# Optimization experiments

Hardware: AMD Instinct MI355X
Metric: run time of the kernel (lower is better)

The kernel has to match this reference:

```python
import jax, jax.numpy as jnp
import numpy as np

N = 50000          # total nodes (100 graphs x 500 nodes)
E = 500000         # total edges
G = 100            # graphs in batch
NODES_PER_GRAPH = 500
N_PROT = 400       # protein nodes per graph (rest are ligand)
H = 128            # hidden_dim
PN, LN, EA = 35, 11, 4
L = 4              # num EGNN layers
EPS = 1e-5


def setup_inputs() -> dict:
    key = jax.random.key(0)
    ks = jax.random.split(key, 40)
    s = 0.1
    inp = {}
    inp["x"] = jax.random.normal(ks[0], (N, PN), jnp.float32)
    inp["pos"] = jax.random.normal(ks[1], (N, 3), jnp.float32)
    inp["edge_index"] = jax.random.randint(ks[2], (2, E), 0, N, jnp.int32)
    inp["edge_attr"] = jax.random.normal(ks[3], (E, EA), jnp.float32)
    node_id = jnp.arange(N, dtype=jnp.int32)
    inp["batch"] = node_id // NODES_PER_GRAPH
    inp["is_protein"] = (node_id % NODES_PER_GRAPH) < N_PROT
    # input projections + batchnorm params
    inp["Wp"] = jax.random.normal(ks[4], (PN, H), jnp.float32) * s
    inp["bp"] = jnp.zeros((H,), jnp.float32)
    inp["Wl"] = jax.random.normal(ks[5], (LN, H), jnp.float32) * s
    inp["bl"] = jnp.zeros((H,), jnp.float32)
    inp["bn_gamma"] = jnp.ones((H,), jnp.float32)
    inp["bn_beta"] = jnp.zeros((H,), jnp.float32)
    # stacked per-layer EGNN params
    din_e = 2 * H + 1 + EA  # 261
    inp["e_w1"] = jax.random.normal(ks[6], (L, din_e, H), jnp.float32) * s
    inp["e_b1"] = jnp.zeros((L, H), jnp.float32)
    inp["e_w2"] = jax.random.normal(ks[7], (L, H, H), jnp.float32) * s
    inp["e_b2"] = jnp.zeros((L, H), jnp.float32)
    inp["c_w1"] = jax.random.normal(ks[8], (L, H, H), jnp.float32) * s
    inp["c_b1"] = jnp.zeros((L, H), jnp.float32)
    inp["c_w2"] = jax.random.normal(ks[9], (L, H, 1), jnp.float32) * s
    inp["n_w1"] = jax.random.normal(ks[10], (L, 2 * H, H), jnp.float32) * s
    inp["n_b1"] = jnp.zeros((L, H), jnp.float32)
    inp["n_w2"] = jax.random.normal(ks[11], (L, H, H), jnp.float32) * s
    inp["n_b2"] = jnp.zeros((L, H), jnp.float32)
    # readout head: 2H -> 128 -> 64 -> 1
    inp["h1_w"] = jax.random.normal(ks[12], (2 * H, 128), jnp.float32) * s
    inp["h1_b"] = jnp.zeros((128,), jnp.float32)
    inp["h2_w"] = jax.random.normal(ks[13], (128, 64), jnp.float32) * s
    inp["h2_b"] = jnp.zeros((64,), jnp.float32)
    inp["h3_w"] = jax.random.normal(ks[14], (64, 1), jnp.float32) * s
    inp["h3_b"] = jnp.zeros((1,), jnp.float32)
    return inp


def reference(x, pos, edge_index, edge_attr, batch, is_protein,
              Wp, bp, Wl, bl, bn_gamma, bn_beta,
              e_w1, e_b1, e_w2, e_b2, c_w1, c_b1, c_w2,
              n_w1, n_b1, n_w2, n_b2,
              h1_w, h1_b, h2_w, h2_b, h3_w, h3_b):
    # --- node projection (protein vs ligand feature slices) ---
    h_prot = x[:, :PN] @ Wp + bp              # [N, H]
    h_lig = x[:, :LN] @ Wl + bl               # [N, H]
    h = jnp.where(is_protein[:, None], h_prot, h_lig)
    # BatchNorm1d (training-mode batch statistics)
    mu = h.mean(axis=0)
    var = h.var(axis=0)
    h = (h - mu) / jnp.sqrt(var + EPS) * bn_gamma + bn_beta

    row, col = edge_index[0], edge_index[1]   # aggregate messages at row (target)
    deg = jax.ops.segment_sum(jnp.ones((row.shape[0],), h.dtype), row, num_segments=N)
    deg = jnp.maximum(deg, 1.0)[:, None]

    for l in range(e_w1.shape[0]):
        rel = pos[row] - pos[col]                                  # [E, 3]
        d2 = jnp.sum(rel * rel, axis=-1, keepdims=True)            # [E, 1]
        feat = jnp.concatenate([h[row], h[col], d2, edge_attr], -1)  # [E, 261]
        m = jax.nn.silu(jax.nn.silu(feat @ e_w1[l] + e_b1[l]) @ e_w2[l] + e_b2[l])  # [E, H]
        # coordinate update (mean aggregation of gated relative positions)
        w = jax.nn.silu(m @ c_w1[l] + c_b1[l]) @ c_w2[l]           # [E, 1]
        pos = pos + jax.ops.segment_sum(rel * w, row, num_segments=N) / deg
        # node update with residual
        agg = jax.ops.segment_sum(m, row, num_segments=N)          # [N, H]
        upd = jax.nn.silu(jnp.concatenate([h, agg], -1) @ n_w1[l] + n_b1[l]) @ n_w2[l] + n_b2[l]
        h = h + upd

    # --- sum||mean pooling per graph ---
    gsum = jax.ops.segment_sum(h, batch, num_segments=G)           # [G, H]
    cnt = jax.ops.segment_sum(jnp.ones((h.shape[0],), h.dtype), batch, num_segments=G)
    gfeat = jnp.concatenate([gsum, gsum / jnp.maximum(cnt, 1.0)[:, None]], -1)  # [G, 2H]

    # --- MLP head (dropout inactive at inference) ---
    z = jax.nn.relu(gfeat @ h1_w + h1_b)
    z = jax.nn.relu(z @ h2_w + h2_b)
    return z @ h3_w + h3_b                                          # [G, 1]
```

## Files before the change

### kernel.cpp

```cpp
#include <hip/hip_runtime.h>
#include <math.h>

#define N_NODES 50000
#define N_EDGES 500000
#define G_GRAPHS 100
#define NPG 500
#define NPROT 400
#define H 128
#define PN 35
#define LN 11
#define DIN 261
#define EB2 32
#define FS2 136
#define T2S 132
#define NBN 64
#define NB2 32
#define CST 264
#define NB 16
#define NCHUNK 49
#define EPSV 1e-5f

typedef __attribute__((ext_vector_type(8))) short bf8_t;
typedef __attribute__((ext_vector_type(4))) short bf4_t;
typedef __attribute__((ext_vector_type(4))) float f4_t;

__device__ __forceinline__ float silu_f(float x) {
    return x / (1.0f + __expf(-x));
}
__device__ __forceinline__ short f2b(float f) {
    __bf16 b = (__bf16)f;
    return __builtin_bit_cast(short, b);
}
__device__ __forceinline__ float b2f(short s) {
    unsigned u = ((unsigned)(unsigned short)s) << 16;
    return __builtin_bit_cast(float, u);
}

__global__ void wprep_frag_kernel(const float* __restrict__ src, short* __restrict__ dstH,
                                  short* __restrict__ dstL, int Ksrc, int nkb, int koff) {
    int idx = blockIdx.x * 256 + threadIdx.x;
    int per_l = nkb * 8 * 64 * 8;
    int total = 4 * per_l;
    if (idx >= total) return;
    int l = idx / per_l;
    int rem = idx - l * per_l;
    int j = rem & 7;
    int lane = (rem >> 3) & 63;
    int nt = (rem >> 9) & 7;
    int kb = rem >> 12;
    int ln = lane & 15, quad = lane >> 4;
    int n = nt * 16 + ln;
    int k = koff + kb * 32 + quad * 8 + j;
    float v = (k < Ksrc) ? src[((size_t)l * Ksrc + k) * H + n] : 0.0f;
    short hi = f2b(v);
    dstH[idx] = hi;
    dstL[idx] = f2b(v - b2f(hi));
}

__global__ void hist_kernel(const int* __restrict__ ei, int* __restrict__ cnt)
{
    int e = blockIdx.x * 256 + threadIdx.x;
    if (e < N_EDGES) atomicAdd(&cnt[ei[e]], 1);
}

__global__ __launch_bounds__(256) void bsum_kernel(const int* __restrict__ cnt, int* __restrict__ bsum)
{
    __shared__ int red[4];
    int tid = threadIdx.x;
    int i0 = blockIdx.x * 1024 + tid * 4;
    int s = 0;
    #pragma unroll
    for (int j = 0; j < 4; j++) {
        int i = i0 + j;
        if (i < N_NODES) s += cnt[i];
    }
    #pragma unroll
    for (int off = 32; off > 0; off >>= 1) s += __shfl_down(s, off, 64);
    if ((tid & 63) == 0) red[tid >> 6] = s;
    __syncthreads();
    if (tid == 0) bsum[blockIdx.x] = red[0] + red[1] + red[2] + red[3];
}

__global__ void scanb_kernel(const int* __restrict__ bsum, int* __restrict__ boff)
{
    if (threadIdx.x == 0) {
        int acc = 0;
        for (int i = 0; i < NCHUNK; i++) { boff[i] = acc; acc += bsum[i]; }
    }
}

__global__ __launch_bounds__(256) void scanc_kernel(const int* __restrict__ cnt,
                                                    const int* __restrict__ boff,
                                                    int* __restrict__ base)
{
    __shared__ int ts[256];
    int tid = threadIdx.x;
    int b = blockIdx.x;
    int i0 = b * 1024 + tid * 4;
    int v0 = (i0 + 0 < N_NODES) ? cnt[i0 + 0] : 0;
    int v1 = (i0 + 1 < N_NODES) ? cnt[i0 + 1] : 0;
    int v2 = (i0 + 2 < N_NODES) ? cnt[i0 + 2] : 0;
    int v3 = (i0 + 3 < N_NODES) ? cnt[i0 + 3] : 0;
    int s0 = v0, s1 = s0 + v1, s2 = s1 + v2, s3 = s2 + v3;
    ts[tid] = s3;
    __syncthreads();
    for (int off = 1; off < 256; off <<= 1) {
        int t = (tid >= off) ? ts[tid - off] : 0;
        __syncthreads();
        ts[tid] += t;
        __syncthreads();
    }
    int excl = ((tid > 0) ? ts[tid - 1] : 0) + boff[b];
    if (i0 + 0 < N_NODES) base[i0 + 0] = excl;
    if (i0 + 1 < N_NODES) base[i0 + 1] = excl + s0;
    if (i0 + 2 < N_NODES) base[i0 + 2] = excl + s1;
    if (i0 + 3 < N_NODES) base[i0 + 3] = excl + s2;
}

__global__ void scatter_kernel(const int* __restrict__ ei, const int* __restrict__ base,
                               int* __restrict__ cursor, int* __restrict__ perm,
                               int* __restrict__ rowsS)
{
    int e = blockIdx.x * 256 + threadIdx.x;
    if (e < N_EDGES) {
        int r = ei[e];
        int p = atomicAdd(&cursor[r], 1);
        int d = base[r] + p;
        perm[d] = e;
        rowsS[d] = r;
    }
}

__global__ void deg_from_cnt_kernel(const int* __restrict__ cnt, float* __restrict__ deg)
{
    int i = blockIdx.x * 256 + threadIdx.x;
    if (i < N_NODES) deg[i] = (float)cnt[i];
}

__global__ __launch_bounds__(128) void proj_kernel(
    const float* __restrict__ x, const float* __restrict__ Wp, const float* __restrict__ bp,
    const float* __restrict__ Wl, const float* __restrict__ bl, float* __restrict__ h)
{
    __shared__ float xs[NB][36];
    int tid = threadIdx.x;
    int n0 = blockIdx.x * NB;
    for (int idx = tid; idx < NB * PN; idx += 128) {
        int n = idx / PN, k = idx % PN;
        xs[n][k] = x[(size_t)(n0 + n) * PN + k];
    }
    __syncthreads();
    for (int n = 0; n < NB; n++) {
        int node = n0 + n;
        bool isp = (node % NPG) < NPROT;
        float acc;
        if (isp) {
            acc = bp[tid];
            for (int k = 0; k < PN; k++) acc = fmaf(xs[n][k], Wp[k * H + tid], acc);
        } else {
            acc = bl[tid];
            for (int k = 0; k < LN; k++) acc = fmaf(xs[n][k], Wl[k * H + tid], acc);
        }
        h[(size_t)node * H + tid] = acc;
    }
}

__global__ __launch_bounds__(128) void bn_stats_kernel(const float* __restrict__ h, float* __restrict__ bnS)
{
    int tid = threadIdx.x;
    size_t base = (size_t)blockIdx.x * NPG * H;
    float s1 = 0.f, s2 = 0.f;
    for (int i = 0; i < NPG; i++) {
        float v = h[base + (size_t)i * H + tid];
        s1 += v; s2 += v * v;
    }
    atomicAdd(&bnS[tid], s1);
    atomicAdd(&bnS[H + tid], s2);
}

__global__ void bn_final_kernel(const float* __restrict__ bnS, const float* __restrict__ gamma,
                                const float* __restrict__ beta, float* __restrict__ bnP)
{
    int j = threadIdx.x;
    float mu = bnS[j] / (float)N_NODES;
    float var = bnS[H + j] / (float)N_NODES - mu * mu;
    float inv = rsqrtf(var + EPSV);
    float sc = gamma[j] * inv;
    bnP[j] = sc;
    bnP[H + j] = beta[j] - mu * sc;
}

__global__ __launch_bounds__(256) void bn_apply_kernel(float* __restrict__ h, const float* __restrict__ bnP)
{
    int idx = blockIdx.x * 256 + threadIdx.x;
    float4 v = ((float4*)h)[idx];
    int j4 = (idx & 31) * 4;
    v.x = fmaf(v.x, bnP[j4 + 0], bnP[H + j4 + 0]);
    v.y = fmaf(v.y, bnP[j4 + 1], bnP[H + j4 + 1]);
    v.z = fmaf(v.z, bnP[j4 + 2], bnP[H + j4 + 2]);
    v.w = fmaf(v.w, bnP[j4 + 3], bnP[H + j4 + 3]);
    ((float4*)h)[idx] = v;
}

__device__ __forceinline__ void mm_hl2(
    const short* fH, const short* fL, int stride,
    const short* __restrict__ WH, const short* __restrict__ WL,
    int nkb, int nt0, int lane, int ln, int quad, f4_t acc[2][2])
{
    #pragma unroll
    for (int mi = 0; mi < 2; mi++)
        #pragma unroll
        for (int ni = 0; ni < 2; ni++) acc[mi][ni] = (f4_t)(0.0f);
    for (int kb = 0; kb < nkb; kb++) {
        int k0 = kb * 32 + quad * 8;
        bf8_t ah0 = *(const bf8_t*)&fH[(ln) * stride + k0];
        bf8_t al0 = *(const bf8_t*)&fL[(ln) * stride + k0];
        bf8_t ah1 = *(const bf8_t*)&fH[(16 + ln) * stride + k0];
        bf8_t al1 = *(const bf8_t*)&fL[(16 + ln) * stride + k0];
        #pragma unroll
        for (int ni = 0; ni < 2; ni++) {
            int off = ((kb * 8 + nt0 + ni) * 64 + lane) * 8;
            bf8_t bh = *(const bf8_t*)&WH[off];
            bf8_t bl = *(const bf8_t*)&WL[off];
            acc[0][ni] = __builtin_amdgcn_mfma_f32_16x16x32_bf16(ah0, bh, acc[0][ni], 0, 0, 0);
            acc[0][ni] = __builtin_amdgcn_mfma_f32_16x16x32_bf16(al0, bh, acc[0][ni], 0, 0, 0);
            acc[0][ni] = __builtin_amdgcn_mfma_f32_16x16x32_bf16(ah0, bl, acc[0][ni], 0, 0, 0);
            acc[1][ni] = __builtin_amdgcn_mfma_f32_16x16x32_bf16(ah1, bh, acc[1][ni], 0, 0, 0);
            acc[1][ni] = __builtin_amdgcn_mfma_f32_16x16x32_bf16(al1, bh, acc[1][ni], 0, 0, 0);
            acc[1][ni] = __builtin_amdgcn_mfma_f32_16x16x32_bf16(ah1, bl, acc[1][ni], 0, 0, 0);
        }
    }
}

__device__ __forceinline__ void mm_h2t(
    const short* fH, int stride,
    const short* __restrict__ WH, const short* __restrict__ WL,
    int nkb, int nt0, int lane, int ln, int quad, f4_t acc[2][2])
{
    #pragma unroll
    for (int mi = 0; mi < 2; mi++)
        #pragma unroll
        for (int ni = 0; ni < 2; ni++) acc[mi][ni] = (f4_t)(0.0f);
    for (int kb = 0; kb < nkb; kb++) {
        int k0 = kb * 32 + quad * 8;
        bf8_t ah0 = *(const bf8_t*)&fH[(ln) * stride + k0];
        bf8_t ah1 = *(const bf8_t*)&fH[(16 + ln) * stride + k0];
        #pragma unroll
        for (int ni = 0; ni < 2; ni++) {
            int off = ((kb * 8 + nt0 + ni) * 64 + lane) * 8;
            bf8_t bh = *(const bf8_t*)&WH[off];
            bf8_t bl = *(const bf8_t*)&WL[off];
            acc[0][ni] = __builtin_amdgcn_mfma_f32_16x16x32_bf16(ah0, bh, acc[0][ni], 0, 0, 0);
            acc[0][ni] = __builtin_amdgcn_mfma_f32_16x16x32_bf16(ah0, bl, acc[0][ni], 0, 0, 0);
            acc[1][ni] = __builtin_amdgcn_mfma_f32_16x16x32_bf16(ah1, bh, acc[1][ni], 0, 0, 0);
            acc[1][ni] = __builtin_amdgcn_mfma_f32_16x16x32_bf16(ah1, bl, acc[1][ni], 0, 0, 0);
        }
    }
}

__device__ __forceinline__ void mm_hl4(
    const short* fH, const short* fL, int stride,
    const short* __restrict__ WH, const short* __restrict__ WL,
    int nkb, int nt, int lane, int ln, int quad, f4_t acc[4])
{
    #pragma unroll
    for (int mi = 0; mi < 4; mi++) acc[mi] = (f4_t)(0.0f);
    for (int kb = 0; kb < nkb; kb++) {
        int k0 = kb * 32 + quad * 8;
        int off = ((kb * 8 + nt) * 64 + lane) * 8;
        bf8_t bh = *(const bf8_t*)&WH[off];
        bf8_t bl = *(const bf8_t*)&WL[off];
        #pragma unroll
        for (int mi = 0; mi < 4; mi++) {
            bf8_t ah = *(const bf8_t*)&fH[(mi * 16 + ln) * stride + k0];
            bf8_t al = *(const bf8_t*)&fL[(mi * 16 + ln) * stride + k0];
            acc[mi] = __builtin_amdgcn_mfma_f32_16x16x32_bf16(ah, bh, acc[mi], 0, 0, 0);
            acc[mi] = __builtin_amdgcn_mfma_f32_16x16x32_bf16(al, bh, acc[mi], 0, 0, 0);
            acc[mi] = __builtin_amdgcn_mfma_f32_16x16x32_bf16(ah, bl, acc[mi], 0, 0, 0);
        }
    }
}

__global__ __launch_bounds__(512, 4) void p12_kernel(
    const float* __restrict__ h,
    const short* __restrict__ Ah, const short* __restrict__ Al,
    const short* __restrict__ Bh, const short* __restrict__ Bl,
    float* __restrict__ P1, float* __restrict__ P2)
{
    __shared__ __align__(16) short fH[NBN * FS2];
    __shared__ __align__(16) short fL[NBN * FS2];
    int tid = threadIdx.x;
    int n0 = blockIdx.x * NBN;

    for (int i = tid; i < NBN * (H / 4); i += 512) {
        int nidx = i >> 5, chunk = i & 31;
        int node = n0 + nidx;
        if (node >= N_NODES) node = N_NODES - 1;
        f4_t v = *(const f4_t*)&h[(size_t)node * H + chunk * 4];
        bf4_t hi, lo;
        #pragma unroll
        for (int j = 0; j < 4; j++) {
            hi[j] = f2b(v[j]);
            lo[j] = f2b(v[j] - b2f(hi[j]));
        }
        *(bf4_t*)&fH[nidx * FS2 + chunk * 4] = hi;
        *(bf4_t*)&fL[nidx * FS2 + chunk * 4] = lo;
    }
    __syncthreads();

    int lane = tid & 63;
    int nt = tid >> 6;
    int ln = lane & 15, quad = lane >> 4;

    f4_t accA[4], accB[4];
    #pragma unroll
    for (int mi = 0; mi < 4; mi++) { accA[mi] = (f4_t)(0.0f); accB[mi] = (f4_t)(0.0f); }
    for (int kb = 0; kb < 4; kb++) {
        int k0 = kb * 32 + quad * 8;
        int off = ((kb * 8 + nt) * 64 + lane) * 8;
        bf8_t bhA = *(const bf8_t*)&Ah[off];
        bf8_t blA = *(const bf8_t*)&Al[off];
        bf8_t bhB = *(const bf8_t*)&Bh[off];
        bf8_t blB = *(const bf8_t*)&Bl[off];
        #pragma unroll
        for (int mi = 0; mi < 4; mi++) {
            bf8_t ah = *(const bf8_t*)&fH[(mi * 16 + ln) * FS2 + k0];
            bf8_t al = *(const bf8_t*)&fL[(mi * 16 + ln) * FS2 + k0];
            accA[mi] = __builtin_amdgcn_mfma_f32_16x16x32_bf16(ah, bhA, accA[mi], 0, 0, 0);
            accA[mi] = __builtin_amdgcn_mfma_f32_16x16x32_bf16(al, bhA, accA[mi], 0, 0, 0);
            accA[mi] = __builtin_amdgcn_mfma_f32_16x16x32_bf16(ah, blA, accA[mi], 0, 0, 0);
            accB[mi] = __builtin_amdgcn_mfma_f32_16x16x32_bf16(ah, bhB, accB[mi], 0, 0, 0);
            accB[mi] = __builtin_amdgcn_mfma_f32_16x16x32_bf16(al, bhB, accB[mi], 0, 0, 0);
            accB[mi] = __builtin_amdgcn_mfma_f32_16x16x32_bf16(ah, blB, accB[mi], 0, 0, 0);
        }
    }
    int n = nt * 16 + ln;
    #pragma unroll
    for (int mi = 0; mi < 4; mi++) {
        #pragma unroll
        for (int r = 0; r < 4; r++) {
            int node = n0 + mi * 16 + quad * 4 + r;
            if (node < N_NODES) {
                P1[(size_t)node * H + n] = accA[mi][r];
                P2[(size_t)node * H + n] = accB[mi][r];
            }
        }
    }
}

__global__ __launch_bounds__(256, 8) void edge_mfma_kernel(
    const float* __restrict__ P1, const float* __restrict__ P2,
    const float* __restrict__ pos,
    const int* __restrict__ ei, const float* __restrict__ eattr,
    const int* __restrict__ perm, const int* __restrict__ rowsS,
    const float* __restrict__ W1c, const float* __restrict__ eb1,
    const short* __restrict__ W2h, const short* __restrict__ W2l,
    const short* __restrict__ W3h, const short* __restrict__ W3l,
    const float* __restrict__ eb2,
    const float* __restrict__ cb1, const float* __restrict__ cw2,
    float* __restrict__ magg, float* __restrict__ pagg)
{
    __shared__ __align__(16) short fHL[2 * EB2 * FS2];
    __shared__ float relS[EB2][3];
    __shared__ float attrS[EB2][5];
    __shared__ float wpart[EB2][4];
    __shared__ int rowS[EB2];
    __shared__ int rowG[EB2];
    __shared__ int colS[EB2];

    short* fH = fHL;
    short* fL = fHL + EB2 * FS2;
    int tid = threadIdx.x;
    int chunk = gridDim.x >> 3;
    int bx = blockIdx.x;
    int bid = (bx & 7) * chunk + (bx >> 3);
    int e0 = bid * EB2;

    if (tid < EB2) {
        int e = e0 + tid;
        int eidx = (e < N_EDGES) ? e : (N_EDGES - 1);
        int ec = perm[eidx];
        int r = rowsS[eidx];
        int c = ei[N_EDGES + ec];
        rowG[tid] = r;
        rowS[tid] = (e < N_EDGES) ? r : -1;
        colS[tid] = c;
        float rx = pos[r * 3 + 0] - pos[c * 3 + 0];
        float ry = pos[r * 3 + 1] - pos[c * 3 + 1];
        float rz = pos[r * 3 + 2] - pos[c * 3 + 2];
        relS[tid][0] = rx; relS[tid][1] = ry; relS[tid][2] = rz;
        attrS[tid][0] = rx * rx + ry * ry + rz * rz;
        attrS[tid][1] = eattr[(size_t)ec * 4 + 0];
        attrS[tid][2] = eattr[(size_t)ec * 4 + 1];
        attrS[tid][3] = eattr[(size_t)ec * 4 + 2];
        attrS[tid][4] = eattr[(size_t)ec * 4 + 3];
    }
    __syncthreads();

    {
        int ch4 = (tid & 31) * 4;
        f4_t bb = *(const f4_t*)&eb1[ch4];
        f4_t w0 = *(const f4_t*)&W1c[0 * H + ch4];
        f4_t w1 = *(const f4_t*)&W1c[1 * H + ch4];
        f4_t w2 = *(const f4_t*)&W1c[2 * H + ch4];
        f4_t w3 = *(const f4_t*)&W1c[3 * H + ch4];
        f4_t w4 = *(const f4_t*)&W1c[4 * H + ch4];
        #pragma unroll
        for (int b = 0; b < 2; b++) {
            int i0 = tid + b * 512;
            int i1 = i0 + 256;
            int ea = i0 >> 5;
            int eb_ = i1 >> 5;
            f4_t p1a = *(const f4_t*)&P1[(size_t)rowG[ea] * H + ch4];
            f4_t p2a = *(const f4_t*)&P2[(size_t)colS[ea] * H + ch4];
            f4_t p1b = *(const f4_t*)&P1[(size_t)rowG[eb_] * H + ch4];
            f4_t p2b = *(const f4_t*)&P2[(size_t)colS[eb_] * H + ch4];
            #pragma unroll
            for (int half = 0; half < 2; half++) {
                int e = half ? eb_ : ea;
                f4_t p1 = half ? p1b : p1a;
                f4_t p2 = half ? p2b : p2a;
                float a0 = attrS[e][0], a1 = attrS[e][1], a2 = attrS[e][2];
                float a3 = attrS[e][3], a4 = attrS[e][4];
                bf4_t hi, lo;
                #pragma unroll
                for (int j = 0; j < 4; j++) {
                    float t = p1[j] + p2[j] + bb[j];
                    t = fmaf(a0, w0[j], t);
                    t = fmaf(a1, w1[j], t);
                    t = fmaf(a2, w2[j], t);
                    t = fmaf(a3, w3[j], t);
                    t = fmaf(a4, w4[j], t);
                    float v = silu_f(t);
                    hi[j] = f2b(v);
                    lo[j] = f2b(v - b2f(hi[j]));
                }
                *(bf4_t*)&fH[e * FS2 + ch4] = hi;
                *(bf4_t*)&fL[e * FS2 + ch4] = lo;
            }
        }
    }
    __syncthreads();

    int lane = tid & 63;
    int wv = tid >> 6;
    int ln = lane & 15, quad = lane >> 4;
    int nt0 = wv * 2;

    f4_t acc[2][2];
    float t2s[2][2][4];

    mm_hl2(fH, fL, FS2, W2h, W2l, 4, nt0, lane, ln, quad, acc);
    #pragma unroll
    for (int ni = 0; ni < 2; ni++) {
        int n = (nt0 + ni) * 16 + ln;
        float bb = eb2[n];
        #pragma unroll
        for (int mi = 0; mi < 2; mi++)
            #pragma unroll
            for (int r = 0; r < 4; r++)
                t2s[mi][ni][r] = silu_f(acc[mi][ni][r] + bb);
    }
    __syncthreads();
    #pragma unroll
    for (int ni = 0; ni < 2; ni++) {
        int n = (nt0 + ni) * 16 + ln;
        #pragma unroll
        for (int mi = 0; mi < 2; mi++) {
            #pragma unroll
            for (int r = 0; r < 4; r++) {
                int m = mi * 16 + quad * 4 + r;
                fH[m * FS2 + n] = f2b(t2s[mi][ni][r]);
            }
        }
    }
    __syncthreads();

    mm_h2t(fH, FS2, W3h, W3l, 4, nt0, lane, ln, quad, acc);
    {
        #pragma unroll
        for (int mi = 0; mi < 2; mi++) {
            #pragma unroll
            for (int r = 0; r < 4; r++) {
                float v = 0.f;
                #pragma unroll
                for (int ni = 0; ni < 2; ni++) {
                    int n = (nt0 + ni) * 16 + ln;
                    v += silu_f(acc[mi][ni][r] + cb1[n]) * cw2[n];
                }
                v += __shfl_xor(v, 1, 64);
                v += __shfl_xor(v, 2, 64);
                v += __shfl_xor(v, 4, 64);
                v += __shfl_xor(v, 8, 64);
                if (ln == 0) wpart[mi * 16 + quad * 4 + r][wv] = v;
            }
        }
    }
    __syncthreads();

    float* t2f = (float*)fHL;
    #pragma unroll
    for (int ni = 0; ni < 2; ni++) {
        int n = (nt0 + ni) * 16 + ln;
        #pragma unroll
        for (int mi = 0; mi < 2; mi++)
            #pragma unroll
            for (int r = 0; r < 4; r++)
                t2f[(mi * 16 + quad * 4 + r) * T2S + n] = t2s[mi][ni][r];
    }
    __syncthreads();

    {
        int ch = tid & 127, seg = tid >> 7;
        int ebeg = seg * 16, eend = ebeg + 16;
        float a2 = 0.f; int cur = -1;
        for (int e2 = ebeg; e2 < eend; e2++) {
            int r2 = rowS[e2];
            float v2 = t2f[e2 * T2S + ch];
            if (r2 != cur) {
                if (cur >= 0) atomicAdd(&magg[(size_t)cur * H + ch], a2);
                cur = r2; a2 = v2;
            } else a2 += v2;
        }
        if (cur >= 0) atomicAdd(&magg[(size_t)cur * H + ch], a2);
    }
    if (tid < 6) {
        int ax = tid % 3, seg = tid / 3;
        int ebeg = seg * 16, eend = ebeg + 16;
        float a2 = 0.f; int cur = -1;
        for (int e2 = ebeg; e2 < eend; e2++) {
            int r2 = rowS[e2];
            float w2 = (wpart[e2][0] + wpart[e2][1] + wpart[e2][2] + wpart[e2][3]) * relS[e2][ax];
            if (r2 != cur) {
                if (cur >= 0) atomicAdd(&pagg[(size_t)cur * 3 + ax], a2);
                cur = r2; a2 = w2;
            } else a2 += w2;
        }
        if (cur >= 0) atomicAdd(&pagg[(size_t)cur * 3 + ax], a2);
    }
}

__global__ __launch_bounds__(256, 8) void node_mfma_kernel(
    float* __restrict__ h, const float* __restrict__ magg,
    const float* __restrict__ pagg, const float* __restrict__ deg,
    float* __restrict__ pos,
    const short* __restrict__ N1h, const short* __restrict__ N1l,
    const short* __restrict__ N2h, const short* __restrict__ N2l,
    const float* __restrict__ nb1, const float* __restrict__ nb2,
    const short* __restrict__ Ah, const short* __restrict__ Al,
    const short* __restrict__ Bh, const short* __restrict__ Bl,
    float* __restrict__ P1, float* __restrict__ P2, int doP)
{
    __shared__ __align__(16) short fH[NB2 * CST];
    __shared__ __align__(16) short fL[NB2 * CST];

    int tid = threadIdx.x;
    int n0 = blockIdx.x * NB2;

    if (tid < NB2 * 3) {
        int n = tid / 3, ax = tid - n * 3;
        int node = n0 + n;
        if (node < N_NODES) {
            float d = fmaxf(deg[node], 1.0f);
            pos[node * 3 + ax] += pagg[node * 3 + ax] / d;
        }
    }

    for (int i = tid; i < 2 * NB2 * (H / 4); i += 256) {
        int rrow = i >> 5, chunk = i & 31;
        int nidx = rrow & (NB2 - 1);
        int node = n0 + nidx;
        if (node >= N_NODES) node = N_NODES - 1;
        const float* src = (rrow < NB2) ? h : magg;
        f4_t v = *(const f4_t*)&src[(size_t)node * H + chunk * 4];
        bf4_t hi, lo;
        #pragma unroll
        for (int j = 0; j < 4; j++) {
            hi[j] = f2b(v[j]);
            lo[j] = f2b(v[j] - b2f(hi[j]));
        }
        int dcol = ((rrow < NB2) ? 0 : H) + chunk * 4;
        *(bf4_t*)&fH[nidx * CST + dcol] = hi;
        *(bf4_t*)&fL[nidx * CST + dcol] = lo;
    }
    __syncthreads();

    int lane = tid & 63;
    int wv = tid >> 6;
    int ln = lane & 15, quad = lane >> 4;
    int nt0 = wv * 2;

    f4_t acc[2][2];
    float u1s[2][2][4];

    mm_hl2(fH, fL, CST, N1h, N1l, 8, nt0, lane, ln, quad, acc);
    #pragma unroll
    for (int ni = 0; ni < 2; ni++) {
        int n = (nt0 + ni) * 16 + ln;
        float bb = nb1[n];
        #pragma unroll
        for (int mi = 0; mi < 2; mi++)
            #pragma unroll
            for (int r = 0; r < 4; r++)
                u1s[mi][ni][r] = silu_f(acc[mi][ni][r] + bb);
    }
    __syncthreads();
    #pragma unroll
    for (int ni = 0; ni < 2; ni++) {
        int n = (nt0 + ni) * 16 + ln;
        #pragma unroll
        for (int mi = 0; mi < 2; mi++) {
            #pragma unroll
            for (int r = 0; r < 4; r++) {
                int m = mi * 16 + quad * 4 + r;
                float v = u1s[mi][ni][r];
                short hi = f2b(v);
                fH[m * CST + n] = hi;
                fL[m * CST + n] = f2b(v - b2f(hi));
            }
        }
    }
    __syncthreads();

    mm_hl2(fH, fL, CST, N2h, N2l, 4, nt0, lane, ln, quad, acc);
    __syncthreads();
    #pragma unroll
    for (int ni = 0; ni < 2; ni++) {
        int n = (nt0 + ni) * 16 + ln;
        float bb = nb2[n];
        #pragma unroll
        for (int mi = 0; mi < 2; mi++) {
            #pragma unroll
            for (int r = 0; r < 4; r++) {
                int m = mi * 16 + quad * 4 + r;
                int node = n0 + m;
                int nc = (node < N_NODES) ? node : (N_NODES - 1);
                float hn = h[(size_t)nc * H + n] + acc[mi][ni][r] + bb;
                if (node < N_NODES) h[(size_t)node * H + n] = hn;
                short hi = f2b(hn);
                fH[m * CST + n] = hi;
                fL[m * CST + n] = f2b(hn - b2f(hi));
            }
        }
    }
    if (!doP) return;
    __syncthreads();

    f4_t accA[2][2], accB[2][2];
    #pragma unroll
    for (int mi = 0; mi < 2; mi++)
        #pragma unroll
        for (int ni = 0; ni < 2; ni++) { accA[mi][ni] = (f4_t)(0.0f); accB[mi][ni] = (f4_t)(0.0f); }
    for (int kb = 0; kb < 4; kb++) {
        int k0 = kb * 32 + quad * 8;
        bf8_t ah0 = *(const bf8_t*)&fH[(ln) * CST + k0];
        bf8_t al0 = *(const bf8_t*)&fL[(ln) * CST + k0];
        bf8_t ah1 = *(const bf8_t*)&fH[(16 + ln) * CST + k0];
        bf8_t al1 = *(const bf8_t*)&fL[(16 + ln) * CST + k0];
        #pragma unroll
        for (int ni = 0; ni < 2; ni++) {
            int off = ((kb * 8 + nt0 + ni) * 64 + lane) * 8;
            bf8_t bhA = *(const bf8_t*)&Ah[off];
            bf8_t blA = *(const bf8_t*)&Al[off];
            bf8_t bhB = *(const bf8_t*)&Bh[off];
            bf8_t blB = *(const bf8_t*)&Bl[off];
            accA[0][ni] = __builtin_amdgcn_mfma_f32_16x16x32_bf16(ah0, bhA, accA[0][ni], 0, 0, 0);
            accA[0][ni] = __builtin_amdgcn_mfma_f32_16x16x32_bf16(al0, bhA, accA[0][ni], 0, 0, 0);
            accA[0][ni] = __builtin_amdgcn_mfma_f32_16x16x32_bf16(ah0, blA, accA[0][ni], 0, 0, 0);
            accA[1][ni] = __builtin_amdgcn_mfma_f32_16x16x32_bf16(ah1, bhA, accA[1][ni], 0, 0, 0);
            accA[1][ni] = __builtin_amdgcn_mfma_f32_16x16x32_bf16(al1, bhA, accA[1][ni], 0, 0, 0);
            accA[1][ni] = __builtin_amdgcn_mfma_f32_16x16x32_bf16(ah1, blA, accA[1][ni], 0, 0, 0);
            accB[0][ni] = __builtin_amdgcn_mfma_f32_16x16x32_bf16(ah0, bhB, accB[0][ni], 0, 0, 0);
            accB[0][ni] = __builtin_amdgcn_mfma_f32_16x16x32_bf16(al0, bhB, accB[0][ni], 0, 0, 0);
            accB[0][ni] = __builtin_amdgcn_mfma_f32_16x16x32_bf16(ah0, blB, accB[0][ni], 0, 0, 0);
            accB[1][ni] = __builtin_amdgcn_mfma_f32_16x16x32_bf16(ah1, bhB, accB[1][ni], 0, 0, 0);
            accB[1][ni] = __builtin_amdgcn_mfma_f32_16x16x32_bf16(al1, bhB, accB[1][ni], 0, 0, 0);
            accB[1][ni] = __builtin_amdgcn_mfma_f32_16x16x32_bf16(ah1, blB, accB[1][ni], 0, 0, 0);
        }
    }
    #pragma unroll
    for (int ni = 0; ni < 2; ni++) {
        int n = (nt0 + ni) * 16 + ln;
        #pragma unroll
        for (int mi = 0; mi < 2; mi++) {
            #pragma unroll
            for (int r = 0; r < 4; r++) {
                int node = n0 + mi * 16 + quad * 4 + r;
                if (node < N_NODES) {
                    P1[(size_t)node * H + n] = accA[mi][ni][r];
                    P2[(size_t)node * H + n] = accB[mi][ni][r];
                }
            }
        }
    }
}

__global__ __launch_bounds__(128) void head_kernel(
    const float* __restrict__ h,
    const float* __restrict__ h1w, const float* __restrict__ h1b,
    const float* __restrict__ h2w, const float* __restrict__ h2b,
    const float* __restrict__ h3w, const float* __restrict__ h3b,
    float* __restrict__ out)
{
    __shared__ float gfeat[256];
    __shared__ float z1[128];
    __shared__ float z2[64];
    int tid = threadIdx.x;
    int g = blockIdx.x;
    size_t base = (size_t)g * NPG * H;
    float s = 0.f;
    for (int i = 0; i < NPG; i++) s += h[base + (size_t)i * H + tid];
    gfeat[tid] = s;
    gfeat[H + tid] = s / (float)NPG;
    __syncthreads();
    float a = h1b[tid];
    for (int k = 0; k < 256; k++) a = fmaf(gfeat[k], h1w[k * H + tid], a);
    z1[tid] = fmaxf(a, 0.0f);
    __syncthreads();
    if (tid < 64) {
        float a2 = h2b[tid];
        for (int k = 0; k < 128; k++) a2 = fmaf(z1[k], h2w[k * 64 + tid], a2);
        z2[tid] = fmaxf(a2, 0.0f);
    }
    __syncthreads();
    if (tid < 64) {
        float v = z2[tid] * h3w[tid];
        #pragma unroll
        for (int off = 32; off > 0; off >>= 1) v += __shfl_xor(v, off, 64);
        if (tid == 0) out[g] = v + h3b[0];
    }
}

extern "C" void kernel_launch(void* const* d_in, const int* in_sizes, int n_in,
                              void* d_out, int out_size, void* d_ws, size_t ws_size,
                              hipStream_t stream) {
    const float* x      = (const float*)d_in[0];
    const float* pos_in = (const float*)d_in[1];
    const int*   ei     = (const int*)d_in[2];
    const float* eattr  = (const float*)d_in[3];
    const float* Wp    = (const float*)d_in[6];
    const float* bp    = (const float*)d_in[7];
    const float* Wl    = (const float*)d_in[8];
    const float* bl    = (const float*)d_in[9];
    const float* gamma = (const float*)d_in[10];
    const float* beta  = (const float*)d_in[11];
    const float* ew1   = (const float*)d_in[12];
    const float* eb1   = (const float*)d_in[13];
    const float* ew2   = (const float*)d_in[14];
    const float* eb2   = (const float*)d_in[15];
    const float* cw1   = (const float*)d_in[16];
    const float* cb1   = (const float*)d_in[17];
    const float* cw2   = (const float*)d_in[18];
    const float* nw1   = (const float*)d_in[19];
    const float* nb1   = (const float*)d_in[20];
    const float* nw2   = (const float*)d_in[21];
    const float* nb2   = (const float*)d_in[22];
    const float* h1w   = (const float*)d_in[23];
    const float* h1b   = (const float*)d_in[24];
    const float* h2w   = (const float*)d_in[25];
    const float* h2b   = (const float*)d_in[26];
    const float* h3w   = (const float*)d_in[27];
    const float* h3b   = (const float*)d_in[28];
    float* out = (float*)d_out;

    float* ws   = (float*)d_ws;
    float* hbuf = ws;
    float* magg = hbuf + (size_t)N_NODES * H;
    float* P1   = magg + (size_t)N_NODES * H;
    float* P2   = P1 + (size_t)N_NODES * H;
    float* posb = P2 + (size_t)N_NODES * H;
    float* pagg = posb + (size_t)N_NODES * 3;
    float* deg  = pagg + (size_t)N_NODES * 3;
    float* bnS  = deg + N_NODES;
    float* bnP  = bnS + 256;
    int* cnt    = (int*)(bnP + 256);
    int* basep  = cnt + N_NODES;
    int* cursor = basep + N_NODES;
    int* perm   = cursor + N_NODES;
    int* rowsS  = perm + N_EDGES;
    int* bsum   = rowsS + N_EDGES;
    int* boff   = bsum + 64;
    int szK4 = 4 * 4 * 4096;
    int szK8 = 4 * 8 * 4096;
    short* W1aH = (short*)(boff + 64);
    short* W1aL = W1aH + szK4;
    short* W1bH = W1aL + szK4;
    short* W1bL = W1bH + szK4;
    short* W2h  = W1bL + szK4;
    short* W2l  = W2h + szK4;
    short* W3h  = W2l + szK4;
    short* W3l  = W3h + szK4;
    short* N1h  = W3l + szK4;
    short* N1l  = N1h + szK8;
    short* N2h  = N1l + szK8;
    short* N2l  = N2h + szK4;

    hipMemcpyAsync(posb, pos_in, (size_t)N_NODES * 3 * sizeof(float),
                   hipMemcpyDeviceToDevice, stream);
    hipMemsetAsync(cnt, 0, N_NODES * sizeof(int), stream);
    hipMemsetAsync(cursor, 0, N_NODES * sizeof(int), stream);
    hipMemsetAsync(bnS, 0, 256 * sizeof(float), stream);

    hist_kernel<<<(N_EDGES + 255) / 256, 256, 0, stream>>>(ei, cnt);
    bsum_kernel<<<NCHUNK, 256, 0, stream>>>(cnt, bsum);
    scanb_kernel<<<1, 64, 0, stream>>>(bsum, boff);
    scanc_kernel<<<NCHUNK, 256, 0, stream>>>(cnt, boff, basep);
    scatter_kernel<<<(N_EDGES + 255) / 256, 256, 0, stream>>>(ei, basep, cursor, perm, rowsS);
    deg_from_cnt_kernel<<<(N_NODES + 255) / 256, 256, 0, stream>>>(cnt, deg);

    wprep_frag_kernel<<<(szK4 + 255) / 256, 256, 0, stream>>>(ew1, W1aH, W1aL, DIN, 4, 0);
    wprep_frag_kernel<<<(szK4 + 255) / 256, 256, 0, stream>>>(ew1, W1bH, W1bL, DIN, 4, H);
    wprep_frag_kernel<<<(szK4 + 255) / 256, 256, 0, stream>>>(ew2, W2h, W2l, H, 4, 0);
    wprep_frag_kernel<<<(szK4 + 255) / 256, 256, 0, stream>>>(cw1, W3h, W3l, H, 4, 0);
    wprep_frag_kernel<<<(szK8 + 255) / 256, 256, 0, stream>>>(nw1, N1h, N1l, 256, 8, 0);
    wprep_frag_kernel<<<(szK4 + 255) / 256, 256, 0, stream>>>(nw2, N2h, N2l, H, 4, 0);

    proj_kernel<<<N_NODES / NB, 128, 0, stream>>>(x, Wp, bp, Wl, bl, hbuf);
    bn_stats_kernel<<<N_NODES / NPG, 128, 0, stream>>>(hbuf, bnS);
    bn_final_kernel<<<1, 128, 0, stream>>>(bnS, gamma, beta, bnP);
    bn_apply_kernel<<<(N_NODES * H / 4) / 256, 256, 0, stream>>>(hbuf, bnP);

    int eblocks = (N_EDGES + EB2 - 1) / EB2;
    int echunk = (eblocks + 7) / 8;
    int eblocks_pad = echunk * 8;
    int nblocks = (N_NODES + NBN - 1) / NBN;
    int nblocks2 = (N_NODES + NB2 - 1) / NB2;

    p12_kernel<<<nblocks, 512, 0, stream>>>(hbuf, W1aH, W1aL, W1bH, W1bL, P1, P2);

    for (int l = 0; l < 4; l++) {
        hipMemsetAsync(magg, 0, (size_t)N_NODES * H * sizeof(float), stream);
        hipMemsetAsync(pagg, 0, (size_t)N_NODES * 3 * sizeof(float), stream);
        edge_mfma_kernel<<<eblocks_pad, 256, 0, stream>>>(
            P1, P2, posb, ei, eattr, perm, rowsS,
            ew1 + (size_t)l * DIN * H + (size_t)2 * H * H,
            eb1 + (size_t)l * H,
            W2h + (size_t)l * 4 * 4096, W2l + (size_t)l * 4 * 4096,
            W3h + (size_t)l * 4 * 4096, W3l + (size_t)l * 4 * 4096,
            eb2 + (size_t)l * H,
            cb1 + (size_t)l * H, cw2 + (size_t)l * H,
            magg, pagg);
        int lp = l + 1;
        node_mfma_kernel<<<nblocks2, 256, 0, stream>>>(
            hbuf, magg, pagg, deg, posb,
            N1h + (size_t)l * 8 * 4096, N1l + (size_t)l * 8 * 4096,
            N2h + (size_t)l * 4 * 4096, N2l + (size_t)l * 4 * 4096,
            nb1 + (size_t)l * H, nb2 + (size_t)l * H,
            W1aH + (size_t)(lp & 3) * 4 * 4096, W1aL + (size_t)(lp & 3) * 4 * 4096,
            W1bH + (size_t)(lp & 3) * 4 * 4096, W1bL + (size_t)(lp & 3) * 4 * 4096,
            P1, P2, (l < 3) ? 1 : 0);
    }

    head_kernel<<<G_GRAPHS, 128, 0, stream>>>(hbuf, h1w, h1b, h2w, h2b, h3w, h3b, out);
}
```

Baseline: 1.266 ms.

## Fuse aggregation-buffer zeroing into node kernel and merge small prep kernels

The per-layer memsets of the edge-message and position aggregation buffers are removed. The node kernel now zeroes those buffers right after reading them, so each layer saves a separate full pass over a 25MB buffer. The six weight-prep launches are merged into one kernel, and the degree conversion moves into the scan kernel, cutting launch count. It also replaces the bf16 hi/lo split and silu division with bit-trick rounding and a hardware reciprocal, which skip NaN handling and change rounding slightly.

```diff
diff --git a/kernel.cpp b/kernel.cpp
--- a/kernel.cpp
+++ b/kernel.cpp
@@ -25,7 +25,7 @@
 typedef __attribute__((ext_vector_type(4))) float f4_t;
 
 __device__ __forceinline__ float silu_f(float x) {
-    return x / (1.0f + __expf(-x));
+    return x * __builtin_amdgcn_rcpf(1.0f + __expf(-x));
 }
 __device__ __forceinline__ short f2b(float f) {
     __bf16 b = (__bf16)f;
@@ -35,15 +35,45 @@
     unsigned u = ((unsigned)(unsigned short)s) << 16;
     return __builtin_bit_cast(float, u);
 }
-
-__global__ void wprep_frag_kernel(const float* __restrict__ src, short* __restrict__ dstH,
-                                  short* __restrict__ dstL, int Ksrc, int nkb, int koff) {
+__device__ __forceinline__ short f2b_fast(float f) {
+    unsigned b = __builtin_bit_cast(unsigned, f);
+    return (short)((b + 0x8000u) >> 16);
+}
+__device__ __forceinline__ short2 split_hl(float v) {
+    unsigned b = __builtin_bit_cast(unsigned, v);
+    unsigned hr = (b + 0x8000u) & 0xFFFF0000u;
+    float lf = v - __builtin_bit_cast(float, hr);
+    unsigned lb = __builtin_bit_cast(unsigned, lf);
+    short2 r;
+    r.x = (short)(hr >> 16);
+    r.y = (short)((lb + 0x8000u) >> 16);
+    return r;
+}
+
+__global__ __launch_bounds__(256) void wprep_all_kernel(
+    const float* __restrict__ ew1, const float* __restrict__ ew2,
+    const float* __restrict__ cw1, const float* __restrict__ nw1,
+    const float* __restrict__ nw2,
+    short* __restrict__ W1aH, short* __restrict__ W1aL,
+    short* __restrict__ W1bH, short* __restrict__ W1bL,
+    short* __restrict__ W2h, short* __restrict__ W2l,
+    short* __restrict__ W3h, short* __restrict__ W3l,
+    short* __restrict__ N1h, short* __restrict__ N1l,
+    short* __restrict__ N2h, short* __restrict__ N2l)
+{
     int idx = blockIdx.x * 256 + threadIdx.x;
+    const float* src; short *dh, *dl; int Ksrc, nkb, koff, base;
+    if (idx < 65536)       { src = ew1; dh = W1aH; dl = W1aL; Ksrc = DIN; nkb = 4; koff = 0; base = 0; }
+    else if (idx < 131072) { src = ew1; dh = W1bH; dl = W1bL; Ksrc = DIN; nkb = 4; koff = H; base = 65536; }
+    else if (idx < 196608) { src = ew2; dh = W2h;  dl = W2l;  Ksrc = H;   nkb = 4; koff = 0; base = 131072; }
+    else if (idx < 262144) { src = cw1; dh = W3h;  dl = W3l;  Ksrc = H;   nkb = 4; koff = 0; base = 196608; }
+    else if (idx < 393216) { src = nw1; dh = N1h;  dl = N1l;  Ksrc = 256; nkb = 8; koff = 0; base = 262144; }
+    else if (idx < 458752) { src = nw2; dh = N2h;  dl = N2l;  Ksrc = H;   nkb = 4; koff = 0; base = 393216; }
+    else return;
+    int rem0 = idx - base;
     int per_l = nkb * 8 * 64 * 8;
-    int total = 4 * per_l;
-    if (idx >= total) return;
-    int l = idx / per_l;
-    int rem = idx - l * per_l;
+    int l = rem0 / per_l;
+    int rem = rem0 - l * per_l;
     int j = rem & 7;
     int lane = (rem >> 3) & 63;
     int nt = (rem >> 9) & 7;
@@ -53,8 +83,8 @@
     int k = koff + kb * 32 + quad * 8 + j;
     float v = (k < Ksrc) ? src[((size_t)l * Ksrc + k) * H + n] : 0.0f;
     short hi = f2b(v);
-    dstH[idx] = hi;
-    dstL[idx] = f2b(v - b2f(hi));
+    dh[rem0] = hi;
+    dl[rem0] = f2b(v - b2f(hi));
 }
 
 __global__ void hist_kernel(const int* __restrict__ ei, int* __restrict__ cnt)
@@ -91,7 +121,8 @@
 
 __global__ __launch_bounds__(256) void scanc_kernel(const int* __restrict__ cnt,
                                                     const int* __restrict__ boff,
-                                                    int* __restrict__ base)
+                                                    int* __restrict__ base,
+                                                    float* __restrict__ deg)
 {
     __shared__ int ts[256];
     int tid = threadIdx.x;
@@ -111,10 +142,10 @@
         __syncthreads();
     }
     int excl = ((tid > 0) ? ts[tid - 1] : 0) + boff[b];
-    if (i0 + 0 < N_NODES) base[i0 + 0] = excl;
-    if (i0 + 1 < N_NODES) base[i0 + 1] = excl + s0;
-    if (i0 + 2 < N_NODES) base[i0 + 2] = excl + s1;
-    if (i0 + 3 < N_NODES) base[i0 + 3] = excl + s2;
+    if (i0 + 0 < N_NODES) { base[i0 + 0] = excl;      deg[i0 + 0] = (float)v0; }
+    if (i0 + 1 < N_NODES) { base[i0 + 1] = excl + s0; deg[i0 + 1] = (float)v1; }
+    if (i0 + 2 < N_NODES) { base[i0 + 2] = excl + s1; deg[i0 + 2] = (float)v2; }
+    if (i0 + 3 < N_NODES) { base[i0 + 3] = excl + s2; deg[i0 + 3] = (float)v3; }
 }
 
 __global__ void scatter_kernel(const int* __restrict__ ei, const int* __restrict__ base,
@@ -129,12 +160,6 @@
         perm[d] = e;
         rowsS[d] = r;
     }
-}
-
-__global__ void deg_from_cnt_kernel(const int* __restrict__ cnt, float* __restrict__ deg)
-{
-    int i = blockIdx.x * 256 + threadIdx.x;
-    if (i < N_NODES) deg[i] = (float)cnt[i];
 }
 
 __global__ __launch_bounds__(128) void proj_kernel(
@@ -257,29 +282,6 @@
     }
 }
 
-__device__ __forceinline__ void mm_hl4(
-    const short* fH, const short* fL, int stride,
-    const short* __restrict__ WH, const short* __restrict__ WL,
-    int nkb, int nt, int lane, int ln, int quad, f4_t acc[4])
-{
-    #pragma unroll
-    for (int mi = 0; mi < 4; mi++) acc[mi] = (f4_t)(0.0f);
-    for (int kb = 0; kb < nkb; kb++) {
-        int k0 = kb * 32 + quad * 8;
-        int off = ((kb * 8 + nt) * 64 + lane) * 8;
-        bf8_t bh = *(const bf8_t*)&WH[off];
-        bf8_t bl = *(const bf8_t*)&WL[off];
-        #pragma unroll
-        for (int mi = 0; mi < 4; mi++) {
-            bf8_t ah = *(const bf8_t*)&fH[(mi * 16 + ln) * stride + k0];
-            bf8_t al = *(const bf8_t*)&fL[(mi * 16 + ln) * stride + k0];
-            acc[mi] = __builtin_amdgcn_mfma_f32_16x16x32_bf16(ah, bh, acc[mi], 0, 0, 0);
-            acc[mi] = __builtin_amdgcn_mfma_f32_16x16x32_bf16(al, bh, acc[mi], 0, 0, 0);
-            acc[mi] = __builtin_amdgcn_mfma_f32_16x16x32_bf16(ah, bl, acc[mi], 0, 0, 0);
-        }
-    }
-}
-
 __global__ __launch_bounds__(512, 4) void p12_kernel(
     const float* __restrict__ h,
     const short* __restrict__ Ah, const short* __restrict__ Al,
@@ -299,8 +301,8 @@
         bf4_t hi, lo;
         #pragma unroll
         for (int j = 0; j < 4; j++) {
-            hi[j] = f2b(v[j]);
-            lo[j] = f2b(v[j] - b2f(hi[j]));
+            short2 s = split_hl(v[j]);
+            hi[j] = s.x; lo[j] = s.y;
         }
         *(bf4_t*)&fH[nidx * FS2 + chunk * 4] = hi;
         *(bf4_t*)&fL[nidx * FS2 + chunk * 4] = lo;
@@ -431,8 +433,8 @@
                     t = fmaf(a3, w3[j], t);
                     t = fmaf(a4, w4[j], t);
                     float v = silu_f(t);
-                    hi[j] = f2b(v);
-                    lo[j] = f2b(v - b2f(hi[j]));
+                    short2 s = split_hl(v);
+                    hi[j] = s.x; lo[j] = s.y;
                 }
                 *(bf4_t*)&fH[e * FS2 + ch4] = hi;
                 *(bf4_t*)&fL[e * FS2 + ch4] = lo;
@@ -469,7 +471,7 @@
             #pragma unroll
             for (int r = 0; r < 4; r++) {
                 int m = mi * 16 + quad * 4 + r;
-                fH[m * FS2 + n] = f2b(t2s[mi][ni][r]);
+                fH[m * FS2 + n] = f2b_fast(t2s[mi][ni][r]);
             }
         }
     }
@@ -540,8 +542,8 @@
 }
 
 __global__ __launch_bounds__(256, 8) void node_mfma_kernel(
-    float* __restrict__ h, const float* __restrict__ magg,
-    const float* __restrict__ pagg, const float* __restrict__ deg,
+    float* __restrict__ h, float* __restrict__ magg,
+    float* __restrict__ pagg, const float* __restrict__ deg,
     float* __restrict__ pos,
     const short* __restrict__ N1h, const short* __restrict__ N1l,
     const short* __restrict__ N2h, const short* __restrict__ N2l,
@@ -562,21 +564,24 @@
         if (node < N_NODES) {
             float d = fmaxf(deg[node], 1.0f);
             pos[node * 3 + ax] += pagg[node * 3 + ax] / d;
+            if (doP) pagg[node * 3 + ax] = 0.0f;
         }
     }
 
     for (int i = tid; i < 2 * NB2 * (H / 4); i += 256) {
         int rrow = i >> 5, chunk = i & 31;
         int nidx = rrow & (NB2 - 1);
-        int node = n0 + nidx;
-        if (node >= N_NODES) node = N_NODES - 1;
+        int node0 = n0 + nidx;
+        int node = (node0 < N_NODES) ? node0 : (N_NODES - 1);
         const float* src = (rrow < NB2) ? h : magg;
         f4_t v = *(const f4_t*)&src[(size_t)node * H + chunk * 4];
+        if (rrow >= NB2 && doP && node0 < N_NODES)
+            *(f4_t*)&magg[(size_t)node * H + chunk * 4] = (f4_t)(0.0f);
         bf4_t hi, lo;
         #pragma unroll
         for (int j = 0; j < 4; j++) {
-            hi[j] = f2b(v[j]);
-            lo[j] = f2b(v[j] - b2f(hi[j]));
+            short2 s = split_hl(v[j]);
+            hi[j] = s.x; lo[j] = s.y;
         }
         int dcol = ((rrow < NB2) ? 0 : H) + chunk * 4;
         *(bf4_t*)&fH[nidx * CST + dcol] = hi;
@@ -612,10 +617,9 @@
             #pragma unroll
             for (int r = 0; r < 4; r++) {
                 int m = mi * 16 + quad * 4 + r;
-                float v = u1s[mi][ni][r];
-                short hi = f2b(v);
-                fH[m * CST + n] = hi;
-                fL[m * CST + n] = f2b(v - b2f(hi));
+                short2 s = split_hl(u1s[mi][ni][r]);
+                fH[m * CST + n] = s.x;
+                fL[m * CST + n] = s.y;
             }
         }
     }
@@ -636,9 +640,9 @@
                 int nc = (node < N_NODES) ? node : (N_NODES - 1);
                 float hn = h[(size_t)nc * H + n] + acc[mi][ni][r] + bb;
                 if (node < N_NODES) h[(size_t)node * H + n] = hn;
-                short hi = f2b(hn);
-                fH[m * CST + n] = hi;
-                fL[m * CST + n] = f2b(hn - b2f(hi));
+                short2 s = split_hl(hn);
+                fH[m * CST + n] = s.x;
+                fL[m * CST + n] = s.y;
             }
         }
     }
@@ -794,25 +798,23 @@
     short* N2h  = N1l + szK8;
     short* N2l  = N2h + szK4;
 
-    hipMemcpyAsync(posb, pos_in, (size_t)N_NODES * 3 * sizeof(float),
-                   hipMemcpyDeviceToDevice, stream);
-    hipMemsetAsync(cnt, 0, N_NODES * sizeof(int), stream);
-    hipMemsetAsync(cursor, 0, N_NODES * sizeof(int), stream);
-    hipMemsetAsync(bnS, 0, 256 * sizeof(float), stream);
+    (void)hipMemcpyAsync(posb, pos_in, (size_t)N_NODES * 3 * sizeof(float),
+                         hipMemcpyDeviceToDevice, stream);
+    (void)hipMemsetAsync(cnt, 0, N_NODES * sizeof(int), stream);
+    (void)hipMemsetAsync(cursor, 0, N_NODES * sizeof(int), stream);
+    (void)hipMemsetAsync(bnS, 0, 256 * sizeof(float), stream);
+    (void)hipMemsetAsync(magg, 0, (size_t)N_NODES * H * sizeof(float), stream);
+    (void)hipMemsetAsync(pagg, 0, (size_t)N_NODES * 3 * sizeof(float), stream);
 
     hist_kernel<<<(N_EDGES + 255) / 256, 256, 0, stream>>>(ei, cnt);
     bsum_kernel<<<NCHUNK, 256, 0, stream>>>(cnt, bsum);
     scanb_kernel<<<1, 64, 0, stream>>>(bsum, boff);
-    scanc_kernel<<<NCHUNK, 256, 0, stream>>>(cnt, boff, basep);
+    scanc_kernel<<<NCHUNK, 256, 0, stream>>>(cnt, boff, basep, deg);
     scatter_kernel<<<(N_EDGES + 255) / 256, 256, 0, stream>>>(ei, basep, cursor, perm, rowsS);
-    deg_from_cnt_kernel<<<(N_NODES + 255) / 256, 256, 0, stream>>>(cnt, deg);
-
-    wprep_frag_kernel<<<(szK4 + 255) / 256, 256, 0, stream>>>(ew1, W1aH, W1aL, DIN, 4, 0);
-    wprep_frag_kernel<<<(szK4 + 255) / 256, 256, 0, stream>>>(ew1, W1bH, W1bL, DIN, 4, H);
-    wprep_frag_kernel<<<(szK4 + 255) / 256, 256, 0, stream>>>(ew2, W2h, W2l, H, 4, 0);
-    wprep_frag_kernel<<<(szK4 + 255) / 256, 256, 0, stream>>>(cw1, W3h, W3l, H, 4, 0);
-    wprep_frag_kernel<<<(szK8 + 255) / 256, 256, 0, stream>>>(nw1, N1h, N1l, 256, 8, 0);
-    wprep_frag_kernel<<<(szK4 + 255) / 256, 256, 0, stream>>>(nw2, N2h, N2l, H, 4, 0);
+
+    wprep_all_kernel<<<458752 / 256, 256, 0, stream>>>(
+        ew1, ew2, cw1, nw1, nw2,
+        W1aH, W1aL, W1bH, W1bL, W2h, W2l, W3h, W3l, N1h, N1l, N2h, N2l);
 
     proj_kernel<<<N_NODES / NB, 128, 0, stream>>>(x, Wp, bp, Wl, bl, hbuf);
     bn_stats_kernel<<<N_NODES / NPG, 128, 0, stream>>>(hbuf, bnS);
@@ -828,8 +830,6 @@
     p12_kernel<<<nblocks, 512, 0, stream>>>(hbuf, W1aH, W1aL, W1bH, W1bL, P1, P2);
 
     for (int l = 0; l < 4; l++) {
-        hipMemsetAsync(magg, 0, (size_t)N_NODES * H * sizeof(float), stream);
-        hipMemsetAsync(pagg, 0, (size_t)N_NODES * 3 * sizeof(float), stream);
         edge_mfma_kernel<<<eblocks_pad, 256, 0, stream>>>(
             P1, P2, posb, ei, eattr, perm, rowsS,
             ew1 + (size_t)l * DIN * H + (size_t)2 * H * H,
```

New measurement: 1.097 ms. 13.3% less time.
